# Kernel tuning notes

Hardware: AMD Instinct MI355X
Metric: run time of the kernel (lower is better)

The kernel has to match this reference:

```python
import jax, jax.numpy as jnp
import numpy as np

B, D = 1, 128
N_STATE, N_EULER, N_FIELD = 4, 3, 1
BUF = 1  # filter_nb // 2


def setup_inputs() -> dict:
    key = jax.random.key(0)
    k1, k2, k3, k4 = jax.random.split(key, 4)
    state0 = jax.random.randint(k1, (B, D, D, D), 0, N_STATE).astype(jnp.float32)
    euler0 = jax.random.uniform(k2, (B, D, D, D, 3), dtype=jnp.float32)
    field0 = jax.random.uniform(k3, (B, D, D, D, 1), dtype=jnp.float32)
    x = jnp.concatenate([state0[..., None], euler0, field0], axis=-1)  # [B,D,D,D,5]
    out = jax.random.normal(k4, (B, D, D, D, N_STATE + N_EULER + N_FIELD), dtype=jnp.float32)
    return {"x": x, "out": out}


def _gather_neighbors(euler0):
    # euler0: [B,D,D,D,3] -> [B,D,D,D,26,3] via 26 fixed shifts (zero-padded, non-periodic)
    d = euler0.shape[1]
    pad = jnp.pad(euler0, ((0, 0), (BUF, BUF), (BUF, BUF), (BUF, BUF), (0, 0)))
    slices = []
    for di in (-1, 0, 1):
        for dj in (-1, 0, 1):
            for dk in (-1, 0, 1):
                if di == 0 and dj == 0 and dk == 0:
                    continue
                slices.append(pad[:, BUF + di:BUF + di + d,
                                  BUF + dj:BUF + dj + d,
                                  BUF + dk:BUF + dk + d, :])
    return jnp.stack(slices, axis=4)


def reference(x, out):
    # Cafe_RNN.decode with n_euler=3 (get_rot is identity).
    state0 = x[..., 0].astype(jnp.int32)                       # [B,D,D,D]
    state1 = jnp.argmax(out[..., :N_STATE], axis=-1).astype(jnp.int32)
    state1 = jnp.where(state0 == 0, 0, state1)

    field1 = out[..., -N_FIELD:]                               # [B,D,D,D,1]
    m_le1 = (state1 <= 1)[..., None]
    m_eq2 = (state1 == 2)[..., None]
    m_eq3 = (state1 == 3)[..., None]
    field1 = jnp.where(m_le1, -1.0, field1)
    field1 = jnp.where(m_eq2, jnp.clip(field1, 0.0, 0.92), field1)
    field1 = jnp.where(m_eq3, 1.0, field1)

    euler1 = x[..., 1:4]
    euler1 = jnp.where(m_le1, -1.0, euler1)

    # Solidification: for cells that just solidified, snap euler to the nearest
    # neighbor euler (min squared distance to the predicted rotation rot1).
    flag_solidify = jnp.logical_and(state0 <= 1, state1 > 1)   # [B,D,D,D]
    rot0_nbs = _gather_neighbors(x[..., 1:4])                  # [B,D,D,D,26,3]
    rot1 = out[..., N_STATE:N_STATE + N_EULER]                 # [B,D,D,D,3]
    dist = jnp.sum(jnp.square(rot0_nbs - rot1[..., None, :]), axis=-1)  # [B,D,D,D,26]
    imin = jnp.argmin(dist, axis=-1)                           # [B,D,D,D]
    chosen = jnp.take_along_axis(rot0_nbs, imin[..., None, None], axis=4)[..., 0, :]
    euler1 = jnp.where(flag_solidify[..., None], chosen, euler1)

    state1f = jax.lax.stop_gradient(state1.astype(x.dtype))
    return jnp.concatenate([state1f[..., None], euler1, field1], axis=-1)
```

## Files before the change

kernel.cpp:

```cpp
#include <hip/hip_runtime.h>

#pragma clang fp contract(off)

#define DD 128
#define NCELL (DD * DD * DD)
#define CPT 4
#define NWAVE (NCELL / 256)

__device__ __forceinline__ void nbr_off(int m, int& di, int& dj, int& dk) {
    const int idx = (m < 13) ? m : m + 1;
    di = idx / 9 - 1;
    dj = (idx / 3) % 3 - 1;
    dk = idx % 3 - 1;
}

__global__ __launch_bounds__(256) void k1_dense(
    const float* __restrict__ x,
    const float* __restrict__ out,
    float* __restrict__ y,
    int* __restrict__ wcnt,
    int* __restrict__ list)
{
    const int t  = blockIdx.x * blockDim.x + threadIdx.x;
    const int n0 = t * CPT;
    if (n0 >= NCELL) return;

    float4 xa[5], oa[8];
    const float4* xp = reinterpret_cast<const float4*>(x) + (size_t)t * 5;
    const float4* op = reinterpret_cast<const float4*>(out) + (size_t)t * 8;
#pragma unroll
    for (int q = 0; q < 5; ++q) xa[q] = xp[q];
#pragma unroll
    for (int q = 0; q < 8; ++q) oa[q] = op[q];

    float xv[20], ov[32], rv[20];
#pragma unroll
    for (int q = 0; q < 5; ++q) {
        xv[q * 4 + 0] = xa[q].x; xv[q * 4 + 1] = xa[q].y;
        xv[q * 4 + 2] = xa[q].z; xv[q * 4 + 3] = xa[q].w;
    }
#pragma unroll
    for (int q = 0; q < 8; ++q) {
        ov[q * 4 + 0] = oa[q].x; ov[q * 4 + 1] = oa[q].y;
        ov[q * 4 + 2] = oa[q].z; ov[q * 4 + 3] = oa[q].w;
    }

    int fmask = 0;
#pragma unroll
    for (int c = 0; c < CPT; ++c) {
        const int s0 = (int)xv[c * 5 + 0];

        float b = ov[c * 8 + 0];
        int   s1 = 0;
        if (ov[c * 8 + 1] > b) { b = ov[c * 8 + 1]; s1 = 1; }
        if (ov[c * 8 + 2] > b) { b = ov[c * 8 + 2]; s1 = 2; }
        if (ov[c * 8 + 3] > b) { b = ov[c * 8 + 3]; s1 = 3; }
        if (s0 == 0) s1 = 0;

        float f1 = ov[c * 8 + 7];
        float e0 = xv[c * 5 + 1], e1 = xv[c * 5 + 2], e2 = xv[c * 5 + 3];

        if (s1 <= 1) {
            f1 = -1.0f; e0 = -1.0f; e1 = -1.0f; e2 = -1.0f;
        } else if (s1 == 2) {
            f1 = fminf(fmaxf(f1, 0.0f), 0.92f);
        } else {
            f1 = 1.0f;
        }

        fmask |= (int)(s0 <= 1 && s1 > 1) << c;

        rv[c * 5 + 0] = (float)s1;
        rv[c * 5 + 1] = e0;
        rv[c * 5 + 2] = e1;
        rv[c * 5 + 3] = e2;
        rv[c * 5 + 4] = f1;
    }

    float4* yp = reinterpret_cast<float4*>(y) + (size_t)t * 5;
#pragma unroll
    for (int q = 0; q < 5; ++q) {
        float4 v;
        v.x = rv[q * 4 + 0]; v.y = rv[q * 4 + 1];
        v.z = rv[q * 4 + 2]; v.w = rv[q * 4 + 3];
        yp[q] = v;
    }

    const int w    = t >> 6;
    const int lane = threadIdx.x & 63;
    const unsigned long long lt = (1ull << lane) - 1ull;
    unsigned total = 0;
#pragma unroll
    for (int c = 0; c < CPT; ++c) {
        const bool flag = (fmask >> c) & 1;
        const unsigned long long mask = __ballot(flag);
        if (flag) {
            const int pos = (int)total + (int)__popcll(mask & lt);
            list[(w << 8) + pos] = n0 + c;
        }
        total += (unsigned)__popcll(mask);
    }
    if (lane == 0) wcnt[w] = (int)total;
}

__global__ __launch_bounds__(256) void k2_gather(
    const float* __restrict__ x,
    const float* __restrict__ out,
    float* __restrict__ y,
    const int* __restrict__ wcnt,
    const int* __restrict__ list)
{
    const int wiw  = threadIdx.x >> 6;
    const int seg  = (blockIdx.x << 2) + wiw;
    const int lane = threadIdx.x & 63;
    const int half = lane & 1;
    const int cnt  = wcnt[seg];

    for (int base = 0; base < cnt; base += 32) {
        const int slot   = base + (lane >> 1);
        const bool active = (slot < cnt);
        const int n = active ? list[(seg << 8) + slot] : 0;

        const int k  = n & (DD - 1);
        const int j  = (n >> 7) & (DD - 1);
        const int i0 = n >> 14;

        const float4 rot = *reinterpret_cast<const float4*>(out + (size_t)n * 8 + 4);
        const double r0 = (double)rot.x, r1 = (double)rot.y, r2 = (double)rot.z;

        float av[13][3];
#pragma unroll
        for (int m2 = 0; m2 < 13; ++m2) {
            int di, dj, dk;
            nbr_off(half * 13 + m2, di, dj, dk);
            const int ii = i0 + di, jj = j + dj, kk = k + dk;
            av[m2][0] = 0.0f; av[m2][1] = 0.0f; av[m2][2] = 0.0f;
            if ((unsigned)ii < (unsigned)DD &&
                (unsigned)jj < (unsigned)DD &&
                (unsigned)kk < (unsigned)DD) {
                const float* p = x + ((size_t)((ii * DD + jj) * DD + kk)) * 5 + 1;
                av[m2][0] = p[0]; av[m2][1] = p[1]; av[m2][2] = p[2];
            }
        }

        double best = 1.0e300;
        float ce0 = 0.0f, ce1 = 0.0f, ce2 = 0.0f;
#pragma unroll
        for (int m2 = 0; m2 < 13; ++m2) {
            const double d0 = (double)av[m2][0] - r0;
            const double d1 = (double)av[m2][1] - r1;
            const double d2 = (double)av[m2][2] - r2;
            const double dist = d0 * d0 + d1 * d1 + d2 * d2;
            if (dist < best) { best = dist; ce0 = av[m2][0]; ce1 = av[m2][1]; ce2 = av[m2][2]; }
        }

        const double obest = __shfl_xor(best, 1, 64);
        const float  oe0   = __shfl_xor(ce0, 1, 64);
        const float  oe1   = __shfl_xor(ce1, 1, 64);
        const float  oe2   = __shfl_xor(ce2, 1, 64);
        const bool take_other = half ? (obest <= best) : (obest < best);
        if (take_other) { ce0 = oe0; ce1 = oe1; ce2 = oe2; }

        if (active && half == 0) {
            float* yp = y + (size_t)n * 5;
            yp[1] = ce0; yp[2] = ce1; yp[3] = ce2;
        }
    }
}

__global__ __launch_bounds__(256) void cafe_rnn_fallback(
    const float* __restrict__ x,
    const float* __restrict__ out,
    float* __restrict__ y)
{
    const int t  = blockIdx.x * blockDim.x + threadIdx.x;
    const int n0 = t * CPT;
    if (n0 >= NCELL) return;

    float4 xa[5], oa[8];
    const float4* xp = reinterpret_cast<const float4*>(x) + (size_t)t * 5;
    const float4* op = reinterpret_cast<const float4*>(out) + (size_t)t * 8;
#pragma unroll
    for (int q = 0; q < 5; ++q) xa[q] = xp[q];
#pragma unroll
    for (int q = 0; q < 8; ++q) oa[q] = op[q];

    float xv[20], ov[32], rv[20];
#pragma unroll
    for (int q = 0; q < 5; ++q) {
        xv[q * 4 + 0] = xa[q].x; xv[q * 4 + 1] = xa[q].y;
        xv[q * 4 + 2] = xa[q].z; xv[q * 4 + 3] = xa[q].w;
    }
#pragma unroll
    for (int q = 0; q < 8; ++q) {
        ov[q * 4 + 0] = oa[q].x; ov[q * 4 + 1] = oa[q].y;
        ov[q * 4 + 2] = oa[q].z; ov[q * 4 + 3] = oa[q].w;
    }

#pragma unroll
    for (int c = 0; c < CPT; ++c) {
        const int s0 = (int)xv[c * 5 + 0];
        float b = ov[c * 8 + 0];
        int   s1 = 0;
        if (ov[c * 8 + 1] > b) { b = ov[c * 8 + 1]; s1 = 1; }
        if (ov[c * 8 + 2] > b) { b = ov[c * 8 + 2]; s1 = 2; }
        if (ov[c * 8 + 3] > b) { b = ov[c * 8 + 3]; s1 = 3; }
        if (s0 == 0) s1 = 0;

        float f1 = ov[c * 8 + 7];
        float e0 = xv[c * 5 + 1], e1 = xv[c * 5 + 2], e2 = xv[c * 5 + 3];
        if (s1 <= 1) { f1 = -1.0f; e0 = -1.0f; e1 = -1.0f; e2 = -1.0f; }
        else if (s1 == 2) { f1 = fminf(fmaxf(f1, 0.0f), 0.92f); }
        else { f1 = 1.0f; }

        if (s0 <= 1 && s1 > 1) {
            const int n = n0 + c;
            const int k = n & (DD - 1);
            const int j = (n >> 7) & (DD - 1);
            const int i = (n >> 14);
            const double r0 = (double)ov[c * 8 + 4];
            const double r1 = (double)ov[c * 8 + 5];
            const double r2 = (double)ov[c * 8 + 6];
            double best = 1.0e300;
            float ce0 = 0.0f, ce1 = 0.0f, ce2 = 0.0f;
#pragma unroll
            for (int m = 0; m < 26; ++m) {
                int di, dj, dk;
                nbr_off(m, di, dj, dk);
                const int ii = i + di, jj = j + dj, kk = k + dk;
                float a0 = 0.0f, a1 = 0.0f, a2 = 0.0f;
                if ((unsigned)ii < (unsigned)DD &&
                    (unsigned)jj < (unsigned)DD &&
                    (unsigned)kk < (unsigned)DD) {
                    const float* p = x + ((size_t)((ii * DD + jj) * DD + kk)) * 5 + 1;
                    a0 = p[0]; a1 = p[1]; a2 = p[2];
                }
                const double d0 = (double)a0 - r0;
                const double d1 = (double)a1 - r1;
                const double d2 = (double)a2 - r2;
                const double dist = d0 * d0 + d1 * d1 + d2 * d2;
                if (dist < best) { best = dist; ce0 = a0; ce1 = a1; ce2 = a2; }
            }
            e0 = ce0; e1 = ce1; e2 = ce2;
        }

        rv[c * 5 + 0] = (float)s1;
        rv[c * 5 + 1] = e0;
        rv[c * 5 + 2] = e1;
        rv[c * 5 + 3] = e2;
        rv[c * 5 + 4] = f1;
    }

    float4* yp = reinterpret_cast<float4*>(y) + (size_t)t * 5;
#pragma unroll
    for (int q = 0; q < 5; ++q) {
        float4 v;
        v.x = rv[q * 4 + 0]; v.y = rv[q * 4 + 1];
        v.z = rv[q * 4 + 2]; v.w = rv[q * 4 + 3];
        yp[q] = v;
    }
}

extern "C" void kernel_launch(void* const* d_in, const int* in_sizes, int n_in,
                              void* d_out, int out_size, void* d_ws, size_t ws_size,
                              hipStream_t stream) {
    const float* x   = (const float*)d_in[0];
    const float* out = (const float*)d_in[1];
    float* y = (float*)d_out;

    const int threads = 256;
    const int blocks1 = NCELL / (threads * CPT);

    const size_t need = (size_t)NWAVE * sizeof(int) + (size_t)NCELL * sizeof(int);
    if (ws_size >= need) {
        int* wcnt = (int*)d_ws;
        int* list = (int*)((char*)d_ws + (size_t)NWAVE * sizeof(int));
        k1_dense<<<blocks1, threads, 0, stream>>>(x, out, y, wcnt, list);
        k2_gather<<<NWAVE / 4, threads, 0, stream>>>(x, out, y, wcnt, list);
    } else {
        cafe_rnn_fallback<<<blocks1, threads, 0, stream>>>(x, out, y);
    }
}
```

Before: 172.3 us.

## Stage k1 inputs through LDS via global_load_lds and write outputs coalesced

New measurement: 171.8 us. Within noise of the previous version (-0.3%).

```diff
diff --git a/kernel.cpp b/kernel.cpp
--- a/kernel.cpp
+++ b/kernel.cpp
@@ -4,14 +4,20 @@
 
 #define DD 128
 #define NCELL (DD * DD * DD)
-#define CPT 4
 #define NWAVE (NCELL / 256)
+#define CELLS_PER_BLOCK 1024
 
 __device__ __forceinline__ void nbr_off(int m, int& di, int& dj, int& dk) {
     const int idx = (m < 13) ? m : m + 1;
     di = idx / 9 - 1;
     dj = (idx / 3) % 3 - 1;
     dk = idx % 3 - 1;
+}
+
+__device__ __forceinline__ void gl_lds16(const float4* g, float4* l) {
+    __builtin_amdgcn_global_load_lds(
+        (const __attribute__((address_space(1))) void*)g,
+        (__attribute__((address_space(3))) void*)l, 16, 0, 0);
 }
 
 __global__ __launch_bounds__(256) void k1_dense(
@@ -21,45 +27,56 @@
     int* __restrict__ wcnt,
     int* __restrict__ list)
 {
-    const int t  = blockIdx.x * blockDim.x + threadIdx.x;
-    const int n0 = t * CPT;
-    if (n0 >= NCELL) return;
-
-    float4 xa[5], oa[8];
-    const float4* xp = reinterpret_cast<const float4*>(x) + (size_t)t * 5;
-    const float4* op = reinterpret_cast<const float4*>(out) + (size_t)t * 8;
-#pragma unroll
-    for (int q = 0; q < 5; ++q) xa[q] = xp[q];
-#pragma unroll
-    for (int q = 0; q < 8; ++q) oa[q] = op[q];
-
-    float xv[20], ov[32], rv[20];
-#pragma unroll
-    for (int q = 0; q < 5; ++q) {
-        xv[q * 4 + 0] = xa[q].x; xv[q * 4 + 1] = xa[q].y;
-        xv[q * 4 + 2] = xa[q].z; xv[q * 4 + 3] = xa[q].w;
+    __shared__ float  x_lds[CELLS_PER_BLOCK * 5];
+    __shared__ float4 o_lds[CELLS_PER_BLOCK * 2];
+
+    const int tid  = threadIdx.x;
+    const int w    = tid >> 6;
+    const int lane = tid & 63;
+    const int blockBase = blockIdx.x * CELLS_PER_BLOCK;
+
+    float4* x_lds4 = reinterpret_cast<float4*>(x_lds);
+    const float4* xg4 = reinterpret_cast<const float4*>(x) + (size_t)blockIdx.x * 1280;
+    const float4* og4 = reinterpret_cast<const float4*>(out) + (size_t)blockIdx.x * 2048;
+
+#pragma unroll
+    for (int q = 0; q < 5; ++q) {
+        const int cx = w * 320 + q * 64;
+        gl_lds16(xg4 + cx + lane, x_lds4 + cx);
     }
 #pragma unroll
     for (int q = 0; q < 8; ++q) {
-        ov[q * 4 + 0] = oa[q].x; ov[q * 4 + 1] = oa[q].y;
-        ov[q * 4 + 2] = oa[q].z; ov[q * 4 + 3] = oa[q].w;
-    }
-
-    int fmask = 0;
-#pragma unroll
-    for (int c = 0; c < CPT; ++c) {
-        const int s0 = (int)xv[c * 5 + 0];
-
-        float b = ov[c * 8 + 0];
+        const int cx = w * 512 + q * 64;
+        gl_lds16(og4 + cx + lane, o_lds + cx);
+    }
+    __syncthreads();
+
+    const unsigned long long lt = (1ull << lane) - 1ull;
+    unsigned total = 0;
+
+#pragma unroll
+    for (int cc = 0; cc < 4; ++cc) {
+        const int c = tid + 256 * cc;
+        const int n = blockBase + c;
+
+        const float s0f = x_lds[5 * c + 0];
+        const float e0i = x_lds[5 * c + 1];
+        const float e1i = x_lds[5 * c + 2];
+        const float e2i = x_lds[5 * c + 3];
+        const float4 lg = o_lds[2 * c + 0];
+        const float4 rf = o_lds[2 * c + 1];
+
+        const int s0 = (int)s0f;
+
+        float b = lg.x;
         int   s1 = 0;
-        if (ov[c * 8 + 1] > b) { b = ov[c * 8 + 1]; s1 = 1; }
-        if (ov[c * 8 + 2] > b) { b = ov[c * 8 + 2]; s1 = 2; }
-        if (ov[c * 8 + 3] > b) { b = ov[c * 8 + 3]; s1 = 3; }
+        if (lg.y > b) { b = lg.y; s1 = 1; }
+        if (lg.z > b) { b = lg.z; s1 = 2; }
+        if (lg.w > b) { b = lg.w; s1 = 3; }
         if (s0 == 0) s1 = 0;
 
-        float f1 = ov[c * 8 + 7];
-        float e0 = xv[c * 5 + 1], e1 = xv[c * 5 + 2], e2 = xv[c * 5 + 3];
-
+        float f1 = rf.w;
+        float e0 = e0i, e1 = e1i, e2 = e2i;
         if (s1 <= 1) {
             f1 = -1.0f; e0 = -1.0f; e1 = -1.0f; e2 = -1.0f;
         } else if (s1 == 2) {
@@ -68,39 +85,31 @@
             f1 = 1.0f;
         }
 
-        fmask |= (int)(s0 <= 1 && s1 > 1) << c;
-
-        rv[c * 5 + 0] = (float)s1;
-        rv[c * 5 + 1] = e0;
-        rv[c * 5 + 2] = e1;
-        rv[c * 5 + 3] = e2;
-        rv[c * 5 + 4] = f1;
-    }
-
-    float4* yp = reinterpret_cast<float4*>(y) + (size_t)t * 5;
-#pragma unroll
-    for (int q = 0; q < 5; ++q) {
-        float4 v;
-        v.x = rv[q * 4 + 0]; v.y = rv[q * 4 + 1];
-        v.z = rv[q * 4 + 2]; v.w = rv[q * 4 + 3];
-        yp[q] = v;
-    }
-
-    const int w    = t >> 6;
-    const int lane = threadIdx.x & 63;
-    const unsigned long long lt = (1ull << lane) - 1ull;
-    unsigned total = 0;
-#pragma unroll
-    for (int c = 0; c < CPT; ++c) {
-        const bool flag = (fmask >> c) & 1;
+        x_lds[5 * c + 0] = (float)s1;
+        x_lds[5 * c + 1] = e0;
+        x_lds[5 * c + 2] = e1;
+        x_lds[5 * c + 3] = e2;
+        x_lds[5 * c + 4] = f1;
+
+        const bool flag = (s0 <= 1 && s1 > 1);
         const unsigned long long mask = __ballot(flag);
         if (flag) {
+            const int gw  = blockIdx.x * 4 + w;
             const int pos = (int)total + (int)__popcll(mask & lt);
-            list[(w << 8) + pos] = n0 + c;
+            list[(gw << 8) + pos] = n;
         }
         total += (unsigned)__popcll(mask);
     }
-    if (lane == 0) wcnt[w] = (int)total;
+    if (lane == 0) wcnt[blockIdx.x * 4 + w] = (int)total;
+
+    __syncthreads();
+
+    float4* yg4 = reinterpret_cast<float4*>(y) + (size_t)blockIdx.x * 1280;
+#pragma unroll
+    for (int q = 0; q < 5; ++q) {
+        const int idx = tid + 256 * q;
+        yg4[idx] = x_lds4[idx];
+    }
 }
 
 __global__ __launch_bounds__(256) void k2_gather(
@@ -174,7 +183,7 @@
     float* __restrict__ y)
 {
     const int t  = blockIdx.x * blockDim.x + threadIdx.x;
-    const int n0 = t * CPT;
+    const int n0 = t * 4;
     if (n0 >= NCELL) return;
 
     float4 xa[5], oa[8];
@@ -198,7 +207,7 @@
     }
 
 #pragma unroll
-    for (int c = 0; c < CPT; ++c) {
+    for (int c = 0; c < 4; ++c) {
         const int s0 = (int)xv[c * 5 + 0];
         float b = ov[c * 8 + 0];
         int   s1 = 0;
@@ -269,15 +278,14 @@
     float* y = (float*)d_out;
 
     const int threads = 256;
-    const int blocks1 = NCELL / (threads * CPT);
 
     const size_t need = (size_t)NWAVE * sizeof(int) + (size_t)NCELL * sizeof(int);
     if (ws_size >= need) {
         int* wcnt = (int*)d_ws;
         int* list = (int*)((char*)d_ws + (size_t)NWAVE * sizeof(int));
-        k1_dense<<<blocks1, threads, 0, stream>>>(x, out, y, wcnt, list);
+        k1_dense<<<NCELL / CELLS_PER_BLOCK, threads, 0, stream>>>(x, out, y, wcnt, list);
         k2_gather<<<NWAVE / 4, threads, 0, stream>>>(x, out, y, wcnt, list);
     } else {
-        cafe_rnn_fallback<<<blocks1, threads, 0, stream>>>(x, out, y);
-    }
-}
+        cafe_rnn_fallback<<<NCELL / (threads * 4), threads, 0, stream>>>(x, out, y);
+    }
+}
```
